# Kernel tuning notes

Hardware: AMD Instinct MI355X
Metric: run time of the kernel (lower is better)

The kernel has to match this reference:

```python
import jax, jax.numpy as jnp
import numpy as np

VOCAB, X_SIZE, H_SIZE, N_CLASSES = 50000, 300, 150, 5
DEPTH = 18                      # complete binary tree, N = 2^(DEPTH+1)-1 nodes
N_NODES = 2 ** (DEPTH + 1) - 1  # 524287
SCALE = 0.05                    # param init scale for numerical sanity


def setup_inputs() -> dict:
    key = jax.random.key(0)
    ks = jax.random.split(key, 8)
    return {
        "x_id": jax.random.randint(ks[0], (N_NODES,), 0, VOCAB, dtype=jnp.int32),
        "emb": jax.random.normal(ks[1], (VOCAB, X_SIZE), jnp.float32) * SCALE,
        "W_iou": jax.random.normal(ks[2], (X_SIZE, 3 * H_SIZE), jnp.float32) * SCALE,
        "U_iou": jax.random.normal(ks[3], (H_SIZE, 3 * H_SIZE), jnp.float32) * SCALE,
        "b_iou": jnp.zeros((3 * H_SIZE,), jnp.float32),
        "W_f": jax.random.normal(ks[4], (X_SIZE, H_SIZE), jnp.float32) * SCALE,
        "U_f": jax.random.normal(ks[5], (H_SIZE, H_SIZE), jnp.float32) * SCALE,
        "b_f": jnp.zeros((H_SIZE,), jnp.float32),
        "W_out": jax.random.normal(ks[6], (H_SIZE, N_CLASSES), jnp.float32) * SCALE,
        "b_out": jnp.zeros((N_CLASSES,), jnp.float32),
    }


def reference(x_id, emb, W_iou, U_iou, b_iou, W_f, U_f, b_f, W_out, b_out):
    # Child-Sum TreeLSTM propagated leaves->root over a complete binary tree
    # stored in heap layout: children of node i are 2i+1, 2i+2.
    N = x_id.shape[0]
    H = U_iou.shape[0]
    depth = int(np.log2(N + 1)) - 1

    x = emb[x_id]  # input_module: embedding lookup  [N, X]
    h = jnp.zeros((N, H), x.dtype)
    c = jnp.zeros((N, H), x.dtype)

    # level-batched topological propagation (19 static levels)
    for lvl in range(depth, -1, -1):
        s, e = 2 ** lvl - 1, 2 ** (lvl + 1) - 1  # node range of this level
        xl = x[s:e]                              # [n_l, X]
        if lvl == depth:  # leaves: zero child state
            h_sum = jnp.zeros((e - s, H), x.dtype)
            fc_sum = jnp.zeros((e - s, H), x.dtype)
        else:
            # children of consecutive nodes are contiguous: [2s+1, 2e+1)
            hc = h[2 * s + 1:2 * e + 1].reshape(e - s, 2, H)
            cc = c[2 * s + 1:2 * e + 1].reshape(e - s, 2, H)
            h_sum = hc.sum(axis=1)               # reduce: sum child h
            # per-child forget gate
            f = jax.nn.sigmoid((xl @ W_f)[:, None, :] + hc @ U_f + b_f)
            fc_sum = (f * cc).sum(axis=1)
        iou = xl @ W_iou + h_sum @ U_iou + b_iou  # [n_l, 3H]
        i, o, u = jnp.split(iou, 3, axis=-1)
        c_new = jax.nn.sigmoid(i) * jnp.tanh(u) + fc_sum
        h_new = jax.nn.sigmoid(o) * jnp.tanh(c_new)
        h = h.at[s:e].set(h_new)
        c = c.at[s:e].set(c_new)

    return h @ W_out + b_out  # output_module: Linear(H, C)  [N, C]
```

## Files before the change

### kernel.cpp

```cpp
#include <hip/hip_runtime.h>
#include <cstdint>

typedef _Float16 f16_t;
typedef __attribute__((ext_vector_type(8))) _Float16 f16x8;
typedef __attribute__((ext_vector_type(4))) _Float16 f16x4;
typedef __attribute__((ext_vector_type(4))) float f32x4;

#define HP      160
#define NCOL    640
#define KXP     320
#define NNODES  524287
#define LEAF_S  262143
#define LEAF_M  262144
#define NVOCAB  50000
#define AST     168

__device__ __forceinline__ float frcp(float x) { return __builtin_amdgcn_rcpf(x); }
__device__ __forceinline__ float sigf(float x) { return frcp(1.0f + __expf(-x)); }
__device__ __forceinline__ float tanhf_(float x) {
  return 1.0f - 2.0f * frcp(1.0f + __expf(2.0f * x));
}
__device__ __forceinline__ f16x8 zero8() {
  f16x8 z;
#pragma unroll
// ... 101 lines not shown
  }
}

__global__ void leafhc_kernel(const f16_t* __restrict__ P, f16_t* __restrict__ Hleaf,
                              f16_t* __restrict__ Cleaf) {
  int idx = blockIdx.x * 256 + threadIdx.x;
  if (idx >= NVOCAB * 80) return;
  int v = idx / 80, t = idx % 80;
  f16x8 pk = *(const f16x8*)&P[(long)v * NCOL + t * 8];
#pragma unroll
  for (int e = 0; e < 2; ++e) {
    float iv = (float)pk[e * 4 + 0], ov = (float)pk[e * 4 + 1], uv = (float)pk[e * 4 + 2];
    float cl = sigf(iv) * tanhf_(uv);
    float hl = sigf(ov) * tanhf_(cl);
    Hleaf[(long)v * HP + t * 2 + e] = (f16_t)hl;
    Cleaf[(long)v * HP + t * 2 + e] = (f16_t)cl;
  }
}

__global__ void oleaf_kernel(const f16_t* __restrict__ Hleaf, const float* __restrict__ W_out,
                             const float* __restrict__ b_out, float* __restrict__ Oleaf) {
  const int tid = threadIdx.x;
  const int row = blockIdx.x * 16 + (tid >> 4), l = tid & 15;
  if (row >= NVOCAB) return;
  float acc[5] = {0, 0, 0, 0, 0};
  for (int j = l; j < 150; j += 16) {
    float hv = (float)Hleaf[(long)row * HP + j];
#pragma unroll
    for (int m = 0; m < 5; ++m) acc[m] += hv * W_out[j * 5 + m];
  }
#pragma unroll
  for (int m = 0; m < 5; ++m) {
    float vv = acc[m];
    vv += __shfl_xor(vv, 1);
    vv += __shfl_xor(vv, 2);
    vv += __shfl_xor(vv, 4);
    vv += __shfl_xor(vv, 8);
    if (l == 0) Oleaf[(long)row * 8 + m] = vv + b_out[m];
  }
}

__global__ void leafout_kernel(const int* __restrict__ x_id, const float* __restrict__ Oleaf,
                               float* __restrict__ out) {
  int leaf = blockIdx.x * 256 + threadIdx.x;
  int xv = x_id[LEAF_S + leaf];
  const float* O = Oleaf + (long)xv * 8;
  float4 o4 = *(const float4*)O;
  float o5 = O[4];
  long base = ((long)LEAF_S + leaf) * 5;
  out[base + 0] = o4.x; out[base + 1] = o4.y; out[base + 2] = o4.z;
  out[base + 3] = o4.w; out[base + 4] = o5;
}

template <bool LEAF>
__global__ __launch_bounds__(256, 3) void fused_kernel(
    const int* __restrict__ x_id, const f16_t* __restrict__ P,
    const f16_t* __restrict__ UreT, const f16_t* __restrict__ Hc,
    const f16_t* __restrict__ Cc, f16_t* __restrict__ Hout,
    f16_t* __restrict__ Cout, const float* __restrict__ W_out,
    const float* __restrict__ b_out, float* __restrict__ out, int s1, int M1) {
  __shared__ __align__(16) f16_t A_sh[64 * AST];
  __shared__ __align__(16) f16_t A2_sh[32 * AST];
  __shared__ __align__(16) f16_t B_sh[128 * 40];
  __shared__ f16_t C_sh[32 * 160];
  const int tid = threadIdx.x;
  const int wid = tid >> 6, lane = tid & 63, l15 = lane & 15, q = lane >> 4;
  const int p0 = blockIdx.x * 32;
  const long childbase = 2L * s1 + 1 + 2 * p0;

#pragma unroll
  for (int i = 0; i < 5; ++i) {
    int ch = tid + 256 * i;
    int r = ch / 20, kc = (ch % 20) * 8;
    f16x8 v;
    if (LEAF) {
      int xv = x_id[childbase + r];
      v = *(const f16x8*)&Hc[(long)xv * HP + kc];
    } else {
      v = *(const f16x8*)&Hc[(long)(2 * p0 + r) * HP + kc];
    }
    *(f16x8*)&A_sh[r * AST + kc] = v;
  }
  __syncthreads();

  int xvp[2], xvl[2], xvr[2];
#pragma unroll
  for (int rr = 0; rr < 2; ++rr) {
    int pl = 8 * wid + 2 * q + rr;
    long pn = (long)s1 + p0 + pl;
    xvp[rr] = x_id[pn];
    if (LEAF) {
      xvl[rr] = x_id[childbase + 2 * pl];
      xvr[rr] = x_id[childbase + 2 * pl + 1];
    }
  }
  float oacc1[2][5] = {};

  for (int jt = 0; jt < 5; ++jt) {
    const int j0 = jt * 32;
    f32x4 acc[4][2];
#pragma unroll
    for (int g = 0; g < 4; ++g)
#pragma unroll
      for (int jh = 0; jh < 2; ++jh) acc[g][jh] = zero4();

    for (int kk = 0; kk < HP; kk += 32) {
#pragma unroll
// ... 106 lines not shown
          }
      }
      __syncthreads();
    }

    if (act2) {
#pragma unroll
      for (int rr = 0; rr < 2; ++rr) {
        const int r = rr * 2;
        const int lr0 = 16 * wid + q * 4 + r;
        const int pl = lr0 >> 1;
        const f16_t* Prp = P + (long)xvp2[rr] * NCOL;
#pragma unroll
        for (int jh = 0; jh < 2; ++jh) {
          const int j = j0 + jh * 16 + l15;
          f16x4 pp = *(const f16x4*)&Prp[j * 4];
          float ipre = (float)pp[0] + acc[0][jh][r] + acc[0][jh][r + 1];
          float opre = (float)pp[1] + acc[1][jh][r] + acc[1][jh][r + 1];
          float upre = (float)pp[2] + acc[2][jh][r] + acc[2][jh][r + 1];
          float pf   = (float)pp[3];
          float fl = sigf(pf + acc[3][jh][r]);
          float fr = sigf(pf + acc[3][jh][r + 1]);
          float clv = (float)C_sh[lr0 * 160 + j];
          float crv = (float)C_sh[(lr0 + 1) * 160 + j];
          float cn = sigf(ipre) * tanhf_(upre) + fl * clv + fr * crv;
          float hn = sigf(opre) * tanhf_(cn);
          Hout[(long)(p02 + pl) * HP + j] = (f16_t)hn;
          Cout[(long)(p02 + pl) * HP + j] = (f16_t)cn;
          int wbase = (j < 150) ? j * 5 : 0;
#pragma unroll
          for (int m = 0; m < 5; ++m) oacc2[rr][m] += hn * W_out[wbase + m];
        }
      }
    }
  }

  if (act2) {
#pragma unroll
    for (int rr = 0; rr < 2; ++rr) {
      int pl = 8 * wid + 2 * q + rr;
#pragma unroll
      for (int m = 0; m < 5; ++m) {
        float v = oacc2[rr][m];
        v += __shfl_xor(v, 1);
        v += __shfl_xor(v, 2);
        v += __shfl_xor(v, 4);
        v += __shfl_xor(v, 8);
        if (l15 == 0) out[((long)s2 + p02 + pl) * 5 + m] = v + b_out[m];
      }
    }
  }
}

__device__ __forceinline__ void level_tile(
    const int* __restrict__ x_id, const f16_t* __restrict__ P,
    const f16_t* __restrict__ UreT, const f16_t* __restrict__ h_child,
    const f16_t* __restrict__ c_child, f16_t* __restrict__ h_par,
    f16_t* __restrict__ c_par, const float* Wo, const float* __restrict__ b_out,
    float* __restrict__ out, int s, int M, int p0, f16_t* A_sh, f16_t* B_sh) {
  const int tid = threadIdx.x;
  const int wid = tid >> 6, lane = tid & 63, l15 = lane & 15, q = lane >> 4;
  int rowsValid = 2 * M - 2 * p0;
  if (rowsValid > 64) rowsValid = 64;

#pragma unroll
  for (int i = 0; i < 5; ++i) {
    int ch = tid + 256 * i;
    int r = ch / 20, kc = (ch % 20) * 8;
    f16x8 v;
    if (r < rowsValid) v = *(const f16x8*)&h_child[(long)(2 * p0 + r) * HP + kc];
    else v = zero8();
    *(f16x8*)&A_sh[r * 184 + kc] = v;
  }
  __syncthreads();

  int xvp[2]; long pnode[2]; int plg[2]; bool valid[2]; int lr0v[2];
#pragma unroll
  for (int rr = 0; rr < 2; ++rr) {
    int lr0 = 16 * wid + q * 4 + rr * 2;
    int pl = lr0 >> 1;
    valid[rr] = (p0 + pl) < M;
    long pn = (long)s + p0 + (valid[rr] ? pl : 0);
    pnode[rr] = pn; plg[rr] = p0 + pl; lr0v[rr] = lr0;
    xvp[rr] = x_id[pn];
  }

  float oacc[2][5];
#pragma unroll
  for (int rr = 0; rr < 2; ++rr)
#pragma unroll
    for (int m = 0; m < 5; ++m) oacc[rr][m] = 0.0f;

  for (int jt = 0; jt < 5; ++jt) {
    const int j0 = jt * 32;
    f32x4 acc[4][2];
#pragma unroll
    for (int g = 0; g < 4; ++g)
#pragma unroll
      for (int jh = 0; jh < 2; ++jh) acc[g][jh] = zero4();

    for (int kk = 0; kk < HP; kk += 32) {
#pragma unroll
      for (int i = 0; i < 2; ++i) {
        int ch = tid + 256 * i;
        int cidx = ch >> 2, kc = (ch & 3) * 8;
        int g = cidx >> 5, jj = cidx & 31;
        int col = g * HP + j0 + jj;
        *(f16x8*)&B_sh[cidx * 40 + kc] = *(const f16x8*)&UreT[col * HP + kk + kc];
      }
      __syncthreads();
      f16x8 af = *(const f16x8*)&A_sh[(16 * wid + l15) * 184 + kk + q * 8];
#pragma unroll
      for (int g = 0; g < 4; ++g)
#pragma unroll
        for (int jh = 0; jh < 2; ++jh) {
          f16x8 bfr = *(const f16x8*)&B_sh[(g * 32 + jh * 16 + l15) * 40 + q * 8];
          acc[g][jh] = __builtin_amdgcn_mfma_f32_16x16x32_f16(af, bfr, acc[g][jh], 0, 0, 0);
        }
      __syncthreads();
    }

#pragma unroll
    for (int rr = 0; rr < 2; ++rr) {
      const int r = rr * 2;
      const f16_t* Prp = P + (long)xvp[rr] * NCOL;
#pragma unroll
      for (int jh = 0; jh < 2; ++jh) {
        const int j = j0 + jh * 16 + l15;
        f16x4 pp = *(const f16x4*)&Prp[j * 4];
        float ipre = (float)pp[0] + acc[0][jh][r] + acc[0][jh][r + 1];
        float opre = (float)pp[1] + acc[1][jh][r] + acc[1][jh][r + 1];
        float upre = (float)pp[2] + acc[2][jh][r] + acc[2][jh][r + 1];
        float pf   = (float)pp[3];
        float fl = sigf(pf + acc[3][jh][r]);
        float fr = sigf(pf + acc[3][jh][r + 1]);
        float clv = valid[rr] ? (float)c_child[(long)(2 * p0 + lr0v[rr]) * HP + j] : 0.0f;
        float crv = valid[rr] ? (float)c_child[(long)(2 * p0 + lr0v[rr] + 1) * HP + j] : 0.0f;
        float cn = sigf(ipre) * tanhf_(upre) + fl * clv + fr * crv;
        float hn = sigf(opre) * tanhf_(cn);
        if (valid[rr]) {
          h_par[(long)plg[rr] * HP + j] = (f16_t)hn;
          c_par[(long)plg[rr] * HP + j] = (f16_t)cn;
        }
#pragma unroll
        for (int m = 0; m < 5; ++m) oacc[rr][m] += hn * Wo[j * 5 + m];
      }
    }
  }

#pragma unroll
  for (int rr = 0; rr < 2; ++rr) {
#pragma unroll
    for (int m = 0; m < 5; ++m) {
      float v = oacc[rr][m];
      v += __shfl_xor(v, 1);
      v += __shfl_xor(v, 2);
      v += __shfl_xor(v, 4);
      v += __shfl_xor(v, 8);
      if (l15 == 0 && valid[rr]) out[pnode[rr] * 5 + m] = v + b_out[m];
    }
  }
}

__global__ __launch_bounds__(256, 4) void tail_kernel(
    const int* __restrict__ x_id, const f16_t* __restrict__ P,
    const f16_t* __restrict__ UreT, f16_t* __restrict__ HA, f16_t* __restrict__ HB,
    f16_t* __restrict__ CA, f16_t* __restrict__ CB, const float* __restrict__ W_out,
    const float* __restrict__ b_out, float* __restrict__ out) {
  __shared__ __align__(16) f16_t A_sh[64 * 184];
  __shared__ __align__(16) f16_t B_sh[128 * 40];
  __shared__ float Wo[800];
  for (int i = threadIdx.x; i < 800; i += 256) Wo[i] = (i < 750) ? W_out[i] : 0.0f;
  for (int lvl = 5; lvl >= 0; --lvl) {
    int s = (1 << lvl) - 1, M = 1 << lvl;
    const f16_t* hc = ((lvl + 1) & 1) ? HA : HB;
    const f16_t* cc = ((lvl + 1) & 1) ? CA : CB;
    f16_t* hp = (lvl & 1) ? HA : HB;
    f16_t* cp = (lvl & 1) ? CA : CB;
    level_tile(x_id, P, UreT, hc, cc, hp, cp, Wo, b_out, out, s, M, 0, A_sh, B_sh);
    __syncthreads();
  }
}

extern "C" void kernel_launch(void* const* d_in, const int* in_sizes, int n_in,
                              void* d_out, int out_size, void* d_ws, size_t ws_size,
                              hipStream_t stream) {
  const int* x_id   = (const int*)d_in[0];
  const float* emb  = (const float*)d_in[1];
  const float* W_iou = (const float*)d_in[2];
  const float* U_iou = (const float*)d_in[3];
  const float* b_iou = (const float*)d_in[4];
  const float* W_f   = (const float*)d_in[5];
  const float* U_f   = (const float*)d_in[6];
  const float* b_f   = (const float*)d_in[7];
  const float* W_out = (const float*)d_in[8];
  const float* b_out = (const float*)d_in[9];
  float* out = (float*)d_out;
  char* ws = (char*)d_ws;

  f16_t* WreT  = (f16_t*)(ws + 0);
  f16_t* UreT  = (f16_t*)(ws + 409600);
  float* bre   = (float*)(ws + 614400);
  f16_t* P     = (f16_t*)(ws + 616960);
  f16_t* Hleaf = (f16_t*)(ws + 64616960);
  f16_t* Cleaf = (f16_t*)(ws + 80616960);
  float* Oleaf = (float*)(ws + 96616960);
  f16_t* HX    = (f16_t*)(ws + 98216960);
  f16_t* HY    = (f16_t*)(ws + 119188480);
  f16_t* CX    = (f16_t*)(ws + 140160000);
  f16_t* CY    = (f16_t*)(ws + 161131520);

  prep_params<<<1203, 256, 0, stream>>>(W_iou, U_iou, b_iou, W_f, U_f, b_f, WreT, UreT, bre);
  gemm_p<<<782, 256, 0, stream>>>(emb, WreT, bre, P);
  leafhc_kernel<<<15625, 256, 0, stream>>>(P, Hleaf, Cleaf);
  oleaf_kernel<<<3125, 256, 0, stream>>>(Hleaf, W_out, b_out, Oleaf);
  leafout_kernel<<<1024, 256, 0, stream>>>(x_id, Oleaf, out);

  fused_kernel<true><<<4096, 256, 0, stream>>>(x_id, P, UreT, Hleaf, Cleaf, HX, CX,
                                               W_out, b_out, out, (1 << 17) - 1, 1 << 17);
  fused_kernel<false><<<1024, 256, 0, stream>>>(x_id, P, UreT, HX, CX, HY, CY,
                                                W_out, b_out, out, (1 << 15) - 1, 1 << 15);
  fused_kernel<false><<<256, 256, 0, stream>>>(x_id, P, UreT, HY, CY, HX, CX,
                                               W_out, b_out, out, (1 << 13) - 1, 1 << 13);
  fused_kernel<false><<<64, 256, 0, stream>>>(x_id, P, UreT, HX, CX, HY, CY,
                                              W_out, b_out, out, (1 << 11) - 1, 1 << 11);
  fused_kernel<false><<<16, 256, 0, stream>>>(x_id, P, UreT, HY, CY, HX, CX,
                                              W_out, b_out, out, (1 << 9) - 1, 1 << 9);
  fused_kernel<false><<<4, 256, 0, stream>>>(x_id, P, UreT, HX, CX, HY, CY,
                                             W_out, b_out, out, (1 << 7) - 1, 1 << 7);
  tail_kernel<<<1, 256, 0, stream>>>(x_id, P, UreT, HX, HY, CX, CY, W_out, b_out, out);

  (void)in_sizes; (void)n_in; (void)out_size; (void)ws_size;
}
```

Measured before the change: 866.8 us.

## Add dedicated single-level kernel for level 17 and re-pair later levels

Result: faster. 823.0 us (-5.1%).

```diff
diff --git a/kernel.cpp b/kernel.cpp
--- a/kernel.cpp
+++ b/kernel.cpp
@@ -177,6 +177,111 @@
   out[base + 3] = o4.w; out[base + 4] = o5;
 }
 
+__global__ __launch_bounds__(256, 3) void level17_kernel(
+    const int* __restrict__ x_id, const f16_t* __restrict__ P,
+    const f16_t* __restrict__ UreT, const f16_t* __restrict__ Hleaf,
+    const f16_t* __restrict__ Cleaf, f16_t* __restrict__ Hout,
+    f16_t* __restrict__ Cout, const float* __restrict__ W_out,
+    const float* __restrict__ b_out, float* __restrict__ out) {
+  __shared__ __align__(16) f16_t A_sh[64 * AST];
+  __shared__ __align__(16) f16_t B_sh[128 * 40];
+  const int tid = threadIdx.x;
+  const int wid = tid >> 6, lane = tid & 63, l15 = lane & 15, q = lane >> 4;
+  const int p0 = blockIdx.x * 32;
+  const int s1 = (1 << 17) - 1;
+  const long childbase = 2L * s1 + 1 + 2 * p0;
+
+#pragma unroll
+  for (int i = 0; i < 5; ++i) {
+    int ch = tid + 256 * i;
+    int r = ch / 20, kc = (ch % 20) * 8;
+    int xv = x_id[childbase + r];
+    *(f16x8*)&A_sh[r * AST + kc] = *(const f16x8*)&Hleaf[(long)xv * HP + kc];
+  }
+  __syncthreads();
+
+  int xvp[2], xvl[2], xvr[2];
+#pragma unroll
+  for (int rr = 0; rr < 2; ++rr) {
+    int pl = 8 * wid + 2 * q + rr;
+    xvp[rr] = x_id[(long)s1 + p0 + pl];
+    xvl[rr] = x_id[childbase + 2 * pl];
+    xvr[rr] = x_id[childbase + 2 * pl + 1];
+  }
+  float oacc[2][5] = {};
+
+  for (int jt = 0; jt < 5; ++jt) {
+    const int j0 = jt * 32;
+    f32x4 acc[4][2];
+#pragma unroll
+    for (int g = 0; g < 4; ++g)
+#pragma unroll
+      for (int jh = 0; jh < 2; ++jh) acc[g][jh] = zero4();
+
+    for (int kk = 0; kk < HP; kk += 32) {
+#pragma unroll
+      for (int i = 0; i < 2; ++i) {
+        int ch = tid + 256 * i;
+        int cidx = ch >> 2, kc = (ch & 3) * 8;
+        int g = cidx >> 5, jj = cidx & 31;
+        int col = g * HP + j0 + jj;
+        *(f16x8*)&B_sh[cidx * 40 + kc] = *(const f16x8*)&UreT[col * HP + kk + kc];
+      }
+      __syncthreads();
+      f16x8 af = *(const f16x8*)&A_sh[(16 * wid + l15) * AST + kk + q * 8];
+#pragma unroll
+      for (int g = 0; g < 4; ++g)
+#pragma unroll
+        for (int jh = 0; jh < 2; ++jh) {
+          f16x8 bfr = *(const f16x8*)&B_sh[(g * 32 + jh * 16 + l15) * 40 + q * 8];
+          acc[g][jh] = __builtin_amdgcn_mfma_f32_16x16x32_f16(af, bfr, acc[g][jh], 0, 0, 0);
+        }
+      __syncthreads();
+    }
+
+#pragma unroll
+    for (int rr = 0; rr < 2; ++rr) {
+      const int r = rr * 2;
+      const int pl = 8 * wid + 2 * q + rr;
+      const f16_t* Prp = P + (long)xvp[rr] * NCOL;
+#pragma unroll
+      for (int jh = 0; jh < 2; ++jh) {
+        const int j = j0 + jh * 16 + l15;
+        f16x4 pp = *(const f16x4*)&Prp[j * 4];
+        float ipre = (float)pp[0] + acc[0][jh][r] + acc[0][jh][r + 1];
+        float opre = (float)pp[1] + acc[1][jh][r] + acc[1][jh][r + 1];
+        float upre = (float)pp[2] + acc[2][jh][r] + acc[2][jh][r + 1];
+        float pf   = (float)pp[3];
+        float fl = sigf(pf + acc[3][jh][r]);
+        float fr = sigf(pf + acc[3][jh][r + 1]);
+        float clv = (float)Cleaf[(long)xvl[rr] * HP + j];
+        float crv = (float)Cleaf[(long)xvr[rr] * HP + j];
+        float cn = sigf(ipre) * tanhf_(upre) + fl * clv + fr * crv;
+        float hn = sigf(opre) * tanhf_(cn);
+        Hout[(long)(p0 + pl) * HP + j] = (f16_t)hn;
+        Cout[(long)(p0 + pl) * HP + j] = (f16_t)cn;
+        int wbase = (j < 150) ? j * 5 : 0;
+#pragma unroll
+        for (int m = 0; m < 5; ++m) oacc[rr][m] += hn * W_out[wbase + m];
+      }
+    }
+  }
+
+#pragma unroll
+  for (int rr = 0; rr < 2; ++rr) {
+    int pl = 8 * wid + 2 * q + rr;
+#pragma unroll
+    for (int m = 0; m < 5; ++m) {
+      float v = oacc[rr][m];
+      v += __shfl_xor(v, 1);
+      v += __shfl_xor(v, 2);
+      v += __shfl_xor(v, 4);
+      v += __shfl_xor(v, 8);
+      if (l15 == 0) out[((long)s1 + p0 + pl) * 5 + m] = v + b_out[m];
+    }
+  }
+}
+
 template <bool LEAF>
 __global__ __launch_bounds__(256, 3) void fused_kernel(
     const int* __restrict__ x_id, const f16_t* __restrict__ P,
@@ -509,7 +614,7 @@
   __shared__ __align__(16) f16_t B_sh[128 * 40];
   __shared__ float Wo[800];
   for (int i = threadIdx.x; i < 800; i += 256) Wo[i] = (i < 750) ? W_out[i] : 0.0f;
-  for (int lvl = 5; lvl >= 0; --lvl) {
+  for (int lvl = 4; lvl >= 0; --lvl) {
     int s = (1 << lvl) - 1, M = 1 << lvl;
     const f16_t* hc = ((lvl + 1) & 1) ? HA : HB;
     const f16_t* cc = ((lvl + 1) & 1) ? CA : CB;
@@ -543,10 +648,22 @@
   f16_t* Hleaf = (f16_t*)(ws + 64616960);
   f16_t* Cleaf = (f16_t*)(ws + 80616960);
   float* Oleaf = (float*)(ws + 96616960);
-  f16_t* HX    = (f16_t*)(ws + 98216960);
-  f16_t* HY    = (f16_t*)(ws + 119188480);
-  f16_t* CX    = (f16_t*)(ws + 140160000);
-  f16_t* CY    = (f16_t*)(ws + 161131520);
+  f16_t* H17   = (f16_t*)(ws + 96616960);
+  f16_t* C17   = (f16_t*)(ws + 138560000);
+  f16_t* H15 = (f16_t*)(ws + 64616960);
+  f16_t* C15 = (f16_t*)(ws + 75102720);
+  f16_t* H13 = (f16_t*)(ws + 96616960);
+  f16_t* C13 = (f16_t*)(ws + 99238400);
+  f16_t* H11 = (f16_t*)(ws + 64616960);
+  f16_t* C11 = (f16_t*)(ws + 65272320);
+  f16_t* H9  = (f16_t*)(ws + 96616960);
+  f16_t* C9  = (f16_t*)(ws + 96780800);
+  f16_t* H7  = (f16_t*)(ws + 64616960);
+  f16_t* C7  = (f16_t*)(ws + 64657920);
+  f16_t* H5  = (f16_t*)(ws + 96616960);
+  f16_t* C5  = (f16_t*)(ws + 96627200);
+  f16_t* HSc = (f16_t*)(ws + 64616960);
+  f16_t* CSc = (f16_t*)(ws + 64627200);
 
   prep_params<<<1203, 256, 0, stream>>>(W_iou, U_iou, b_iou, W_f, U_f, b_f, WreT, UreT, bre);
   gemm_p<<<782, 256, 0, stream>>>(emb, WreT, bre, P);
@@ -554,19 +671,21 @@
   oleaf_kernel<<<3125, 256, 0, stream>>>(Hleaf, W_out, b_out, Oleaf);
   leafout_kernel<<<1024, 256, 0, stream>>>(x_id, Oleaf, out);
 
-  fused_kernel<true><<<4096, 256, 0, stream>>>(x_id, P, UreT, Hleaf, Cleaf, HX, CX,
-                                               W_out, b_out, out, (1 << 17) - 1, 1 << 17);
-  fused_kernel<false><<<1024, 256, 0, stream>>>(x_id, P, UreT, HX, CX, HY, CY,
-                                                W_out, b_out, out, (1 << 15) - 1, 1 << 15);
-  fused_kernel<false><<<256, 256, 0, stream>>>(x_id, P, UreT, HY, CY, HX, CX,
-                                               W_out, b_out, out, (1 << 13) - 1, 1 << 13);
-  fused_kernel<false><<<64, 256, 0, stream>>>(x_id, P, UreT, HX, CX, HY, CY,
-                                              W_out, b_out, out, (1 << 11) - 1, 1 << 11);
-  fused_kernel<false><<<16, 256, 0, stream>>>(x_id, P, UreT, HY, CY, HX, CX,
-                                              W_out, b_out, out, (1 << 9) - 1, 1 << 9);
-  fused_kernel<false><<<4, 256, 0, stream>>>(x_id, P, UreT, HX, CX, HY, CY,
-                                             W_out, b_out, out, (1 << 7) - 1, 1 << 7);
-  tail_kernel<<<1, 256, 0, stream>>>(x_id, P, UreT, HX, HY, CX, CY, W_out, b_out, out);
+  level17_kernel<<<4096, 256, 0, stream>>>(x_id, P, UreT, Hleaf, Cleaf, H17, C17,
+                                           W_out, b_out, out);
+  fused_kernel<false><<<2048, 256, 0, stream>>>(x_id, P, UreT, H17, C17, H15, C15,
+                                                W_out, b_out, out, (1 << 16) - 1, 1 << 16);
+  fused_kernel<false><<<512, 256, 0, stream>>>(x_id, P, UreT, H15, C15, H13, C13,
+                                               W_out, b_out, out, (1 << 14) - 1, 1 << 14);
+  fused_kernel<false><<<128, 256, 0, stream>>>(x_id, P, UreT, H13, C13, H11, C11,
+                                               W_out, b_out, out, (1 << 12) - 1, 1 << 12);
+  fused_kernel<false><<<32, 256, 0, stream>>>(x_id, P, UreT, H11, C11, H9, C9,
+                                              W_out, b_out, out, (1 << 10) - 1, 1 << 10);
+  fused_kernel<false><<<8, 256, 0, stream>>>(x_id, P, UreT, H9, C9, H7, C7,
+                                             W_out, b_out, out, (1 << 8) - 1, 1 << 8);
+  fused_kernel<false><<<2, 256, 0, stream>>>(x_id, P, UreT, H7, C7, H5, C5,
+                                             W_out, b_out, out, (1 << 6) - 1, 1 << 6);
+  tail_kernel<<<1, 256, 0, stream>>>(x_id, P, UreT, H5, HSc, C5, CSc, W_out, b_out, out);
 
   (void)in_sizes; (void)n_in; (void)out_size; (void)ws_size;
 }
```

## Split tree levels into per-level kernels with node-per-block small-level path

Applied to the files above, without the earlier changes.

After: 991.3 us. 1.14x slower.

```diff
diff --git a/kernel.cpp b/kernel.cpp
--- a/kernel.cpp
+++ b/kernel.cpp
@@ -177,6 +177,111 @@
   out[base + 3] = o4.w; out[base + 4] = o5;
 }
 
+__global__ __launch_bounds__(256, 3) void level17_kernel(
+    const int* __restrict__ x_id, const f16_t* __restrict__ P,
+    const f16_t* __restrict__ UreT, const f16_t* __restrict__ Hleaf,
+    const f16_t* __restrict__ Cleaf, f16_t* __restrict__ Hout,
+    f16_t* __restrict__ Cout, const float* __restrict__ W_out,
+    const float* __restrict__ b_out, float* __restrict__ out) {
+  __shared__ __align__(16) f16_t A_sh[64 * AST];
+  __shared__ __align__(16) f16_t B_sh[128 * 40];
+  const int tid = threadIdx.x;
+  const int wid = tid >> 6, lane = tid & 63, l15 = lane & 15, q = lane >> 4;
+  const int p0 = blockIdx.x * 32;
+  const int s1 = (1 << 17) - 1;
+  const long childbase = 2L * s1 + 1 + 2 * p0;
+
+#pragma unroll
+  for (int i = 0; i < 5; ++i) {
+    int ch = tid + 256 * i;
+    int r = ch / 20, kc = (ch % 20) * 8;
+    int xv = x_id[childbase + r];
+    *(f16x8*)&A_sh[r * AST + kc] = *(const f16x8*)&Hleaf[(long)xv * HP + kc];
+  }
+  __syncthreads();
+
+  int xvp[2], xvl[2], xvr[2];
+#pragma unroll
+  for (int rr = 0; rr < 2; ++rr) {
+    int pl = 8 * wid + 2 * q + rr;
+    xvp[rr] = x_id[(long)s1 + p0 + pl];
+    xvl[rr] = x_id[childbase + 2 * pl];
+    xvr[rr] = x_id[childbase + 2 * pl + 1];
+  }
+  float oacc[2][5] = {};
+
+  for (int jt = 0; jt < 5; ++jt) {
+    const int j0 = jt * 32;
+    f32x4 acc[4][2];
+#pragma unroll
+    for (int g = 0; g < 4; ++g)
+#pragma unroll
+      for (int jh = 0; jh < 2; ++jh) acc[g][jh] = zero4();
+
+    for (int kk = 0; kk < HP; kk += 32) {
+#pragma unroll
+      for (int i = 0; i < 2; ++i) {
+        int ch = tid + 256 * i;
+        int cidx = ch >> 2, kc = (ch & 3) * 8;
+        int g = cidx >> 5, jj = cidx & 31;
+        int col = g * HP + j0 + jj;
+        *(f16x8*)&B_sh[cidx * 40 + kc] = *(const f16x8*)&UreT[col * HP + kk + kc];
+      }
+      __syncthreads();
+      f16x8 af = *(const f16x8*)&A_sh[(16 * wid + l15) * AST + kk + q * 8];
+#pragma unroll
+      for (int g = 0; g < 4; ++g)
+#pragma unroll
+        for (int jh = 0; jh < 2; ++jh) {
+          f16x8 bfr = *(const f16x8*)&B_sh[(g * 32 + jh * 16 + l15) * 40 + q * 8];
+          acc[g][jh] = __builtin_amdgcn_mfma_f32_16x16x32_f16(af, bfr, acc[g][jh], 0, 0, 0);
+        }
+      __syncthreads();
+    }
+
+#pragma unroll
+    for (int rr = 0; rr < 2; ++rr) {
+      const int r = rr * 2;
+      const int pl = 8 * wid + 2 * q + rr;
+      const f16_t* Prp = P + (long)xvp[rr] * NCOL;
+#pragma unroll
+      for (int jh = 0; jh < 2; ++jh) {
+        const int j = j0 + jh * 16 + l15;
+        f16x4 pp = *(const f16x4*)&Prp[j * 4];
+        float ipre = (float)pp[0] + acc[0][jh][r] + acc[0][jh][r + 1];
+        float opre = (float)pp[1] + acc[1][jh][r] + acc[1][jh][r + 1];
+        float upre = (float)pp[2] + acc[2][jh][r] + acc[2][jh][r + 1];
+        float pf   = (float)pp[3];
+        float fl = sigf(pf + acc[3][jh][r]);
+        float fr = sigf(pf + acc[3][jh][r + 1]);
+        float clv = (float)Cleaf[(long)xvl[rr] * HP + j];
+        float crv = (float)Cleaf[(long)xvr[rr] * HP + j];
+        float cn = sigf(ipre) * tanhf_(upre) + fl * clv + fr * crv;
+        float hn = sigf(opre) * tanhf_(cn);
+        Hout[(long)(p0 + pl) * HP + j] = (f16_t)hn;
+        Cout[(long)(p0 + pl) * HP + j] = (f16_t)cn;
+        int wbase = (j < 150) ? j * 5 : 0;
+#pragma unroll
+        for (int m = 0; m < 5; ++m) oacc[rr][m] += hn * W_out[wbase + m];
+      }
+    }
+  }
+
+#pragma unroll
+  for (int rr = 0; rr < 2; ++rr) {
+    int pl = 8 * wid + 2 * q + rr;
+#pragma unroll
+    for (int m = 0; m < 5; ++m) {
+      float v = oacc[rr][m];
+      v += __shfl_xor(v, 1);
+      v += __shfl_xor(v, 2);
+      v += __shfl_xor(v, 4);
+      v += __shfl_xor(v, 8);
+      if (l15 == 0) out[((long)s1 + p0 + pl) * 5 + m] = v + b_out[m];
+    }
+  }
+}
+
 template <bool LEAF>
 __global__ __launch_bounds__(256, 3) void fused_kernel(
     const int* __restrict__ x_id, const f16_t* __restrict__ P,
@@ -390,133 +495,78 @@
   }
 }
 
-__device__ __forceinline__ void level_tile(
+__global__ __launch_bounds__(256) void small_level(
     const int* __restrict__ x_id, const f16_t* __restrict__ P,
-    const f16_t* __restrict__ UreT, const f16_t* __restrict__ h_child,
-    const f16_t* __restrict__ c_child, f16_t* __restrict__ h_par,
-    f16_t* __restrict__ c_par, const float* Wo, const float* __restrict__ b_out,
-    float* __restrict__ out, int s, int M, int p0, f16_t* A_sh, f16_t* B_sh) {
+    const f16_t* __restrict__ UreT, const f16_t* __restrict__ Hc,
+    const f16_t* __restrict__ Cc, f16_t* __restrict__ Hp, f16_t* __restrict__ Cp,
+    const float* __restrict__ W_out, const float* __restrict__ b_out,
+    float* __restrict__ out, int s) {
+  __shared__ __align__(16) f16_t hlr[320];
+  __shared__ float partial[4][5];
   const int tid = threadIdx.x;
-  const int wid = tid >> 6, lane = tid & 63, l15 = lane & 15, q = lane >> 4;
-  int rowsValid = 2 * M - 2 * p0;
-  if (rowsValid > 64) rowsValid = 64;
-
-#pragma unroll
-  for (int i = 0; i < 5; ++i) {
-    int ch = tid + 256 * i;
-    int r = ch / 20, kc = (ch % 20) * 8;
-    f16x8 v;
-    if (r < rowsValid) v = *(const f16x8*)&h_child[(long)(2 * p0 + r) * HP + kc];
-    else v = zero8();
-    *(f16x8*)&A_sh[r * 184 + kc] = v;
-  }
+  const int p = blockIdx.x;
+  const long cb = (long)(2 * p) * HP;
+
+  if (tid < 40) *(f16x8*)&hlr[tid * 8] = *(const f16x8*)&Hc[cb + tid * 8];
   __syncthreads();
 
-  int xvp[2]; long pnode[2]; int plg[2]; bool valid[2]; int lr0v[2];
-#pragma unroll
-  for (int rr = 0; rr < 2; ++rr) {
-    int lr0 = 16 * wid + q * 4 + rr * 2;
-    int pl = lr0 >> 1;
-    valid[rr] = (p0 + pl) < M;
-    long pn = (long)s + p0 + (valid[rr] ? pl : 0);
-    pnode[rr] = pn; plg[rr] = p0 + pl; lr0v[rr] = lr0;
-    xvp[rr] = x_id[pn];
-  }
-
-  float oacc[2][5];
-#pragma unroll
-  for (int rr = 0; rr < 2; ++rr)
-#pragma unroll
-    for (int m = 0; m < 5; ++m) oacc[rr][m] = 0.0f;
-
-  for (int jt = 0; jt < 5; ++jt) {
-    const int j0 = jt * 32;
-    f32x4 acc[4][2];
-#pragma unroll
-    for (int g = 0; g < 4; ++g)
-#pragma unroll
-      for (int jh = 0; jh < 2; ++jh) acc[g][jh] = zero4();
-
-    for (int kk = 0; kk < HP; kk += 32) {
-#pragma unroll
-      for (int i = 0; i < 2; ++i) {
-        int ch = tid + 256 * i;
-        int cidx = ch >> 2, kc = (ch & 3) * 8;
-        int g = cidx >> 5, jj = cidx & 31;
-        int col = g * HP + j0 + jj;
-        *(f16x8*)&B_sh[cidx * 40 + kc] = *(const f16x8*)&UreT[col * HP + kk + kc];
-      }
-      __syncthreads();
-      f16x8 af = *(const f16x8*)&A_sh[(16 * wid + l15) * 184 + kk + q * 8];
-#pragma unroll
-      for (int g = 0; g < 4; ++g)
-#pragma unroll
-        for (int jh = 0; jh < 2; ++jh) {
-          f16x8 bfr = *(const f16x8*)&B_sh[(g * 32 + jh * 16 + l15) * 40 + q * 8];
-          acc[g][jh] = __builtin_amdgcn_mfma_f32_16x16x32_f16(af, bfr, acc[g][jh], 0, 0, 0);
-        }
-      __syncthreads();
-    }
-
-#pragma unroll
-    for (int rr = 0; rr < 2; ++rr) {
-      const int r = rr * 2;
-      const f16_t* Prp = P + (long)xvp[rr] * NCOL;
-#pragma unroll
-      for (int jh = 0; jh < 2; ++jh) {
-        const int j = j0 + jh * 16 + l15;
-        f16x4 pp = *(const f16x4*)&Prp[j * 4];
-        float ipre = (float)pp[0] + acc[0][jh][r] + acc[0][jh][r + 1];
-        float opre = (float)pp[1] + acc[1][jh][r] + acc[1][jh][r + 1];
-        float upre = (float)pp[2] + acc[2][jh][r] + acc[2][jh][r + 1];
-        float pf   = (float)pp[3];
-        float fl = sigf(pf + acc[3][jh][r]);
-        float fr = sigf(pf + acc[3][jh][r + 1]);
-        float clv = valid[rr] ? (float)c_child[(long)(2 * p0 + lr0v[rr]) * HP + j] : 0.0f;
-        float crv = valid[rr] ? (float)c_child[(long)(2 * p0 + lr0v[rr] + 1) * HP + j] : 0.0f;
-        float cn = sigf(ipre) * tanhf_(upre) + fl * clv + fr * crv;
-        float hn = sigf(opre) * tanhf_(cn);
-        if (valid[rr]) {
-          h_par[(long)plg[rr] * HP + j] = (f16_t)hn;
-          c_par[(long)plg[rr] * HP + j] = (f16_t)cn;
-        }
-#pragma unroll
-        for (int m = 0; m < 5; ++m) oacc[rr][m] += hn * Wo[j * 5 + m];
-      }
-    }
-  }
-
-#pragma unroll
-  for (int rr = 0; rr < 2; ++rr) {
-#pragma unroll
-    for (int m = 0; m < 5; ++m) {
-      float v = oacc[rr][m];
-      v += __shfl_xor(v, 1);
-      v += __shfl_xor(v, 2);
-      v += __shfl_xor(v, 4);
-      v += __shfl_xor(v, 8);
-      if (l15 == 0 && valid[rr]) out[pnode[rr] * 5 + m] = v + b_out[m];
-    }
-  }
-}
-
-__global__ __launch_bounds__(256, 4) void tail_kernel(
-    const int* __restrict__ x_id, const f16_t* __restrict__ P,
-    const f16_t* __restrict__ UreT, f16_t* __restrict__ HA, f16_t* __restrict__ HB,
-    f16_t* __restrict__ CA, f16_t* __restrict__ CB, const float* __restrict__ W_out,
-    const float* __restrict__ b_out, float* __restrict__ out) {
-  __shared__ __align__(16) f16_t A_sh[64 * 184];
-  __shared__ __align__(16) f16_t B_sh[128 * 40];
-  __shared__ float Wo[800];
-  for (int i = threadIdx.x; i < 800; i += 256) Wo[i] = (i < 750) ? W_out[i] : 0.0f;
-  for (int lvl = 5; lvl >= 0; --lvl) {
-    int s = (1 << lvl) - 1, M = 1 << lvl;
-    const f16_t* hc = ((lvl + 1) & 1) ? HA : HB;
-    const f16_t* cc = ((lvl + 1) & 1) ? CA : CB;
-    f16_t* hp = (lvl & 1) ? HA : HB;
-    f16_t* cp = (lvl & 1) ? CA : CB;
-    level_tile(x_id, P, UreT, hc, cc, hp, cp, Wo, b_out, out, s, M, 0, A_sh, B_sh);
-    __syncthreads();
+  const int j = tid;
+  float ai = 0.f, ao = 0.f, au = 0.f, afl = 0.f, afr = 0.f;
+  float hn = 0.f;
+  float contrib[5] = {0.f, 0.f, 0.f, 0.f, 0.f};
+  if (j < HP) {
+    const f16_t* Ui = &UreT[(long)(0 * HP + j) * HP];
+    const f16_t* Uo = &UreT[(long)(1 * HP + j) * HP];
+    const f16_t* Uu = &UreT[(long)(2 * HP + j) * HP];
+    const f16_t* Uf = &UreT[(long)(3 * HP + j) * HP];
+#pragma unroll 5
+    for (int k8 = 0; k8 < 19; ++k8) {
+      f16x8 hl8 = *(const f16x8*)&hlr[k8 * 8];
+      f16x8 hr8 = *(const f16x8*)&hlr[160 + k8 * 8];
+      f16x8 ui8 = *(const f16x8*)&Ui[k8 * 8];
+      f16x8 uo8 = *(const f16x8*)&Uo[k8 * 8];
+      f16x8 uu8 = *(const f16x8*)&Uu[k8 * 8];
+      f16x8 uf8 = *(const f16x8*)&Uf[k8 * 8];
+#pragma unroll
+      for (int e = 0; e < 8; ++e) {
+        float hlv = (float)hl8[e], hrv = (float)hr8[e];
+        float hsv = hlv + hrv;
+        ai  += hsv * (float)ui8[e];
+        ao  += hsv * (float)uo8[e];
+        au  += hsv * (float)uu8[e];
+        afl += hlv * (float)uf8[e];
+        afr += hrv * (float)uf8[e];
+      }
+    }
+    int xv = x_id[(long)s + p];
+    f16x4 pp = *(const f16x4*)&P[(long)xv * NCOL + j * 4];
+    float ipre = (float)pp[0] + ai;
+    float opre = (float)pp[1] + ao;
+    float upre = (float)pp[2] + au;
+    float pf   = (float)pp[3];
+    float fl = sigf(pf + afl), fr = sigf(pf + afr);
+    float clv = (float)Cc[cb + j];
+    float crv = (float)Cc[cb + HP + j];
+    float cn = sigf(ipre) * tanhf_(upre) + fl * clv + fr * crv;
+    hn = sigf(opre) * tanhf_(cn);
+    Hp[(long)p * HP + j] = (f16_t)hn;
+    Cp[(long)p * HP + j] = (f16_t)cn;
+    int wbase = (j < 150) ? j * 5 : 0;
+#pragma unroll
+    for (int m = 0; m < 5; ++m) contrib[m] = hn * W_out[wbase + m];
+  }
+  const int w = tid >> 6, l = tid & 63;
+#pragma unroll
+  for (int m = 0; m < 5; ++m) {
+    float v = contrib[m];
+    v += __shfl_xor(v, 1);  v += __shfl_xor(v, 2);  v += __shfl_xor(v, 4);
+    v += __shfl_xor(v, 8);  v += __shfl_xor(v, 16); v += __shfl_xor(v, 32);
+    if (l == 0) partial[w][m] = v;
+  }
+  __syncthreads();
+  if (tid < 5) {
+    float v = partial[0][tid] + partial[1][tid] + partial[2][tid] + partial[3][tid];
+    out[((long)s + p) * 5 + tid] = v + b_out[tid];
   }
 }
 
@@ -543,10 +593,19 @@
   f16_t* Hleaf = (f16_t*)(ws + 64616960);
   f16_t* Cleaf = (f16_t*)(ws + 80616960);
   float* Oleaf = (float*)(ws + 96616960);
-  f16_t* HX    = (f16_t*)(ws + 98216960);
-  f16_t* HY    = (f16_t*)(ws + 119188480);
-  f16_t* CX    = (f16_t*)(ws + 140160000);
-  f16_t* CY    = (f16_t*)(ws + 161131520);
+  f16_t* H17   = (f16_t*)(ws + 96616960);
+  f16_t* C17   = (f16_t*)(ws + 138560000);
+  f16_t* H15 = (f16_t*)(ws + 64616960);
+  f16_t* C15 = (f16_t*)(ws + 75102720);
+  f16_t* H13 = (f16_t*)(ws + 96616960);
+  f16_t* C13 = (f16_t*)(ws + 99238400);
+  char* vb = ws + 85588480;
+  f16_t* VH[13]; f16_t* VC[13];
+  for (int L = 12; L >= 0; --L) {
+    size_t rows = (size_t)1 << L;
+    VH[L] = (f16_t*)vb; vb += rows * 320;
+    VC[L] = (f16_t*)vb; vb += rows * 320;
+  }
 
   prep_params<<<1203, 256, 0, stream>>>(W_iou, U_iou, b_iou, W_f, U_f, b_f, WreT, UreT, bre);
   gemm_p<<<782, 256, 0, stream>>>(emb, WreT, bre, P);
@@ -554,19 +613,19 @@
   oleaf_kernel<<<3125, 256, 0, stream>>>(Hleaf, W_out, b_out, Oleaf);
   leafout_kernel<<<1024, 256, 0, stream>>>(x_id, Oleaf, out);
 
-  fused_kernel<true><<<4096, 256, 0, stream>>>(x_id, P, UreT, Hleaf, Cleaf, HX, CX,
-                                               W_out, b_out, out, (1 << 17) - 1, 1 << 17);
-  fused_kernel<false><<<1024, 256, 0, stream>>>(x_id, P, UreT, HX, CX, HY, CY,
-                                                W_out, b_out, out, (1 << 15) - 1, 1 << 15);
-  fused_kernel<false><<<256, 256, 0, stream>>>(x_id, P, UreT, HY, CY, HX, CX,
-                                               W_out, b_out, out, (1 << 13) - 1, 1 << 13);
-  fused_kernel<false><<<64, 256, 0, stream>>>(x_id, P, UreT, HX, CX, HY, CY,
-                                              W_out, b_out, out, (1 << 11) - 1, 1 << 11);
-  fused_kernel<false><<<16, 256, 0, stream>>>(x_id, P, UreT, HY, CY, HX, CX,
-                                              W_out, b_out, out, (1 << 9) - 1, 1 << 9);
-  fused_kernel<false><<<4, 256, 0, stream>>>(x_id, P, UreT, HX, CX, HY, CY,
-                                             W_out, b_out, out, (1 << 7) - 1, 1 << 7);
-  tail_kernel<<<1, 256, 0, stream>>>(x_id, P, UreT, HX, HY, CX, CY, W_out, b_out, out);
+  level17_kernel<<<4096, 256, 0, stream>>>(x_id, P, UreT, Hleaf, Cleaf, H17, C17,
+                                           W_out, b_out, out);
+  fused_kernel<false><<<2048, 256, 0, stream>>>(x_id, P, UreT, H17, C17, H15, C15,
+                                                W_out, b_out, out, (1 << 16) - 1, 1 << 16);
+  fused_kernel<false><<<512, 256, 0, stream>>>(x_id, P, UreT, H15, C15, H13, C13,
+                                               W_out, b_out, out, (1 << 14) - 1, 1 << 14);
+  small_level<<<4096, 256, 0, stream>>>(x_id, P, UreT, H13, C13, VH[12], VC[12],
+                                        W_out, b_out, out, (1 << 12) - 1);
+  for (int L = 11; L >= 0; --L) {
+    small_level<<<(1 << L), 256, 0, stream>>>(x_id, P, UreT, VH[L + 1], VC[L + 1],
+                                              VH[L], VC[L], W_out, b_out, out,
+                                              (1 << L) - 1);
+  }
 
   (void)in_sizes; (void)n_in; (void)out_size; (void)ws_size;
 }
```

## Replace two-level fused kernels with per-level kernels staging full UreT tile in LDS

Applied to the files above, without the earlier changes.

New measurement: 884.4 us. 1.02x slower.

```diff
diff --git a/kernel.cpp b/kernel.cpp
--- a/kernel.cpp
+++ b/kernel.cpp
@@ -178,6 +178,142 @@
 }
 
 template <bool LEAF>
+__device__ __forceinline__ void level_tile_fk(
+    const int* __restrict__ x_id, const f16_t* __restrict__ P,
+    const f16_t* __restrict__ UreT, const f16_t* __restrict__ Hc,
+    const f16_t* __restrict__ Cc, f16_t* __restrict__ Hp, f16_t* __restrict__ Cp,
+    const float* __restrict__ W_out, const float* __restrict__ b_out,
+    float* __restrict__ out, int s, int M, int p0, f16_t* A_sh, f16_t* B_sh) {
+  const int tid = threadIdx.x;
+  const int wid = tid >> 6, lane = tid & 63, l15 = lane & 15, q = lane >> 4;
+  const long childbase = 2L * s + 1 + 2 * p0;
+  int rowsValid = 2 * M - 2 * p0;
+  if (rowsValid > 64) rowsValid = 64;
+
+#pragma unroll
+  for (int i = 0; i < 5; ++i) {
+    int ch = tid + 256 * i;
+    int r = ch / 20, kc = (ch % 20) * 8;
+    f16x8 v;
+    if (LEAF) {
+      int xv = x_id[childbase + r];
+      v = *(const f16x8*)&Hc[(long)xv * HP + kc];
+    } else {
+      v = (r < rowsValid) ? *(const f16x8*)&Hc[(long)(2 * p0 + r) * HP + kc] : zero8();
+    }
+    *(f16x8*)&A_sh[r * AST + kc] = v;
+  }
+
+  int xvp[2], xvl[2], xvr[2]; bool valid[2];
+#pragma unroll
+  for (int rr = 0; rr < 2; ++rr) {
+    int pl = 8 * wid + 2 * q + rr;
+    valid[rr] = (p0 + pl) < M;
+    long pn = (long)s + p0 + (valid[rr] ? pl : 0);
+    xvp[rr] = x_id[pn];
+    if (LEAF) {
+      xvl[rr] = x_id[childbase + 2 * pl];
+      xvr[rr] = x_id[childbase + 2 * pl + 1];
+    }
+  }
+  float oacc[2][5] = {};
+
+  for (int jt = 0; jt < 5; ++jt) {
+    const int j0 = jt * 32;
+#pragma unroll
+    for (int i = 0; i < 10; ++i) {
+      int ch = tid + 256 * i;
+      int r = ch / 20, kc = (ch % 20) * 8;
+      int col = (r >> 5) * HP + j0 + (r & 31);
+      *(f16x8*)&B_sh[r * AST + kc] = *(const f16x8*)&UreT[(long)col * HP + kc];
+    }
+    __syncthreads();
+
+    f32x4 acc[4][2];
+#pragma unroll
+    for (int g = 0; g < 4; ++g)
+#pragma unroll
+      for (int jh = 0; jh < 2; ++jh) acc[g][jh] = zero4();
+
+#pragma unroll
+    for (int kk = 0; kk < HP; kk += 32) {
+      f16x8 af = *(const f16x8*)&A_sh[(16 * wid + l15) * AST + kk + q * 8];
+#pragma unroll
+      for (int g = 0; g < 4; ++g)
+#pragma unroll
+        for (int jh = 0; jh < 2; ++jh) {
+          f16x8 bfr = *(const f16x8*)&B_sh[(g * 32 + jh * 16 + l15) * AST + kk + q * 8];
+          acc[g][jh] = __builtin_amdgcn_mfma_f32_16x16x32_f16(af, bfr, acc[g][jh], 0, 0, 0);
+        }
+    }
+    __syncthreads();
+
+#pragma unroll
+    for (int rr = 0; rr < 2; ++rr) {
+      const int r = rr * 2;
+      const int lr0 = 16 * wid + q * 4 + r;
+      const int pl = lr0 >> 1;
+      const f16_t* Prp = P + (long)xvp[rr] * NCOL;
+#pragma unroll
+      for (int jh = 0; jh < 2; ++jh) {
+        const int j = j0 + jh * 16 + l15;
+        f16x4 pp = *(const f16x4*)&Prp[j * 4];
+        float ipre = (float)pp[0] + acc[0][jh][r] + acc[0][jh][r + 1];
+        float opre = (float)pp[1] + acc[1][jh][r] + acc[1][jh][r + 1];
+        float upre = (float)pp[2] + acc[2][jh][r] + acc[2][jh][r + 1];
+        float pf   = (float)pp[3];
+        float fl = sigf(pf + acc[3][jh][r]);
+        float fr = sigf(pf + acc[3][jh][r + 1]);
+        float clv, crv;
+        if (LEAF) {
+          clv = (float)Cc[(long)xvl[rr] * HP + j];
+          crv = (float)Cc[(long)xvr[rr] * HP + j];
+        } else {
+          clv = valid[rr] ? (float)Cc[(long)(2 * p0 + lr0) * HP + j] : 0.0f;
+          crv = valid[rr] ? (float)Cc[(long)(2 * p0 + lr0 + 1) * HP + j] : 0.0f;
+        }
+        float cn = sigf(ipre) * tanhf_(upre) + fl * clv + fr * crv;
+        float hn = sigf(opre) * tanhf_(cn);
+        if (valid[rr]) {
+          Hp[(long)(p0 + pl) * HP + j] = (f16_t)hn;
+          Cp[(long)(p0 + pl) * HP + j] = (f16_t)cn;
+        }
+        int wbase = (j < 150) ? j * 5 : 0;
+#pragma unroll
+        for (int m = 0; m < 5; ++m) oacc[rr][m] += hn * W_out[wbase + m];
+      }
+    }
+  }
+
+#pragma unroll
+  for (int rr = 0; rr < 2; ++rr) {
+    int pl = 8 * wid + 2 * q + rr;
+#pragma unroll
+    for (int m = 0; m < 5; ++m) {
+      float v = oacc[rr][m];
+      v += __shfl_xor(v, 1);
+      v += __shfl_xor(v, 2);
+      v += __shfl_xor(v, 4);
+      v += __shfl_xor(v, 8);
+      if (l15 == 0 && valid[rr]) out[((long)s + p0 + pl) * 5 + m] = v + b_out[m];
+    }
+  }
+}
+
+template <bool LEAF>
+__global__ __launch_bounds__(256, 2) void level_kernel(
+    const int* __restrict__ x_id, const f16_t* __restrict__ P,
+    const f16_t* __restrict__ UreT, const f16_t* __restrict__ Hc,
+    const f16_t* __restrict__ Cc, f16_t* __restrict__ Hout,
+    f16_t* __restrict__ Cout, const float* __restrict__ W_out,
+    const float* __restrict__ b_out, float* __restrict__ out, int s, int M) {
+  __shared__ __align__(16) f16_t A_sh[64 * AST];
+  __shared__ __align__(16) f16_t B_sh[128 * AST];
+  level_tile_fk<LEAF>(x_id, P, UreT, Hc, Cc, Hout, Cout, W_out, b_out, out,
+                      s, M, blockIdx.x * 32, A_sh, B_sh);
+}
+
+template <bool LEAF>
 __global__ __launch_bounds__(256, 3) void fused_kernel(
     const int* __restrict__ x_id, const f16_t* __restrict__ P,
     const f16_t* __restrict__ UreT, const f16_t* __restrict__ Hc,
@@ -390,132 +526,21 @@
   }
 }
 
-__device__ __forceinline__ void level_tile(
-    const int* __restrict__ x_id, const f16_t* __restrict__ P,
-    const f16_t* __restrict__ UreT, const f16_t* __restrict__ h_child,
-    const f16_t* __restrict__ c_child, f16_t* __restrict__ h_par,
-    f16_t* __restrict__ c_par, const float* Wo, const float* __restrict__ b_out,
-    float* __restrict__ out, int s, int M, int p0, f16_t* A_sh, f16_t* B_sh) {
-  const int tid = threadIdx.x;
-  const int wid = tid >> 6, lane = tid & 63, l15 = lane & 15, q = lane >> 4;
-  int rowsValid = 2 * M - 2 * p0;
-  if (rowsValid > 64) rowsValid = 64;
-
-#pragma unroll
-  for (int i = 0; i < 5; ++i) {
-    int ch = tid + 256 * i;
-    int r = ch / 20, kc = (ch % 20) * 8;
-    f16x8 v;
-    if (r < rowsValid) v = *(const f16x8*)&h_child[(long)(2 * p0 + r) * HP + kc];
-    else v = zero8();
-    *(f16x8*)&A_sh[r * 184 + kc] = v;
-  }
-  __syncthreads();
-
-  int xvp[2]; long pnode[2]; int plg[2]; bool valid[2]; int lr0v[2];
-#pragma unroll
-  for (int rr = 0; rr < 2; ++rr) {
-    int lr0 = 16 * wid + q * 4 + rr * 2;
-    int pl = lr0 >> 1;
-    valid[rr] = (p0 + pl) < M;
-    long pn = (long)s + p0 + (valid[rr] ? pl : 0);
-    pnode[rr] = pn; plg[rr] = p0 + pl; lr0v[rr] = lr0;
-    xvp[rr] = x_id[pn];
-  }
-
-  float oacc[2][5];
-#pragma unroll
-  for (int rr = 0; rr < 2; ++rr)
-#pragma unroll
-    for (int m = 0; m < 5; ++m) oacc[rr][m] = 0.0f;
-
-  for (int jt = 0; jt < 5; ++jt) {
-    const int j0 = jt * 32;
-    f32x4 acc[4][2];
-#pragma unroll
-    for (int g = 0; g < 4; ++g)
-#pragma unroll
-      for (int jh = 0; jh < 2; ++jh) acc[g][jh] = zero4();
-
-    for (int kk = 0; kk < HP; kk += 32) {
-#pragma unroll
-      for (int i = 0; i < 2; ++i) {
-        int ch = tid + 256 * i;
-        int cidx = ch >> 2, kc = (ch & 3) * 8;
-        int g = cidx >> 5, jj = cidx & 31;
-        int col = g * HP + j0 + jj;
-        *(f16x8*)&B_sh[cidx * 40 + kc] = *(const f16x8*)&UreT[col * HP + kk + kc];
-      }
-      __syncthreads();
-      f16x8 af = *(const f16x8*)&A_sh[(16 * wid + l15) * 184 + kk + q * 8];
-#pragma unroll
-      for (int g = 0; g < 4; ++g)
-#pragma unroll
-        for (int jh = 0; jh < 2; ++jh) {
-          f16x8 bfr = *(const f16x8*)&B_sh[(g * 32 + jh * 16 + l15) * 40 + q * 8];
-          acc[g][jh] = __builtin_amdgcn_mfma_f32_16x16x32_f16(af, bfr, acc[g][jh], 0, 0, 0);
-        }
-      __syncthreads();
-    }
-
-#pragma unroll
-    for (int rr = 0; rr < 2; ++rr) {
-      const int r = rr * 2;
-      const f16_t* Prp = P + (long)xvp[rr] * NCOL;
-#pragma unroll
-      for (int jh = 0; jh < 2; ++jh) {
-        const int j = j0 + jh * 16 + l15;
-        f16x4 pp = *(const f16x4*)&Prp[j * 4];
-        float ipre = (float)pp[0] + acc[0][jh][r] + acc[0][jh][r + 1];
-        float opre = (float)pp[1] + acc[1][jh][r] + acc[1][jh][r + 1];
-        float upre = (float)pp[2] + acc[2][jh][r] + acc[2][jh][r + 1];
-        float pf   = (float)pp[3];
-        float fl = sigf(pf + acc[3][jh][r]);
-        float fr = sigf(pf + acc[3][jh][r + 1]);
-        float clv = valid[rr] ? (float)c_child[(long)(2 * p0 + lr0v[rr]) * HP + j] : 0.0f;
-        float crv = valid[rr] ? (float)c_child[(long)(2 * p0 + lr0v[rr] + 1) * HP + j] : 0.0f;
-        float cn = sigf(ipre) * tanhf_(upre) + fl * clv + fr * crv;
-        float hn = sigf(opre) * tanhf_(cn);
-        if (valid[rr]) {
-          h_par[(long)plg[rr] * HP + j] = (f16_t)hn;
-          c_par[(long)plg[rr] * HP + j] = (f16_t)cn;
-        }
-#pragma unroll
-        for (int m = 0; m < 5; ++m) oacc[rr][m] += hn * Wo[j * 5 + m];
-      }
-    }
-  }
-
-#pragma unroll
-  for (int rr = 0; rr < 2; ++rr) {
-#pragma unroll
-    for (int m = 0; m < 5; ++m) {
-      float v = oacc[rr][m];
-      v += __shfl_xor(v, 1);
-      v += __shfl_xor(v, 2);
-      v += __shfl_xor(v, 4);
-      v += __shfl_xor(v, 8);
-      if (l15 == 0 && valid[rr]) out[pnode[rr] * 5 + m] = v + b_out[m];
-    }
-  }
-}
-
-__global__ __launch_bounds__(256, 4) void tail_kernel(
+__global__ __launch_bounds__(256, 2) void tail_fk(
     const int* __restrict__ x_id, const f16_t* __restrict__ P,
     const f16_t* __restrict__ UreT, f16_t* __restrict__ HA, f16_t* __restrict__ HB,
     f16_t* __restrict__ CA, f16_t* __restrict__ CB, const float* __restrict__ W_out,
     const float* __restrict__ b_out, float* __restrict__ out) {
-  __shared__ __align__(16) f16_t A_sh[64 * 184];
-  __shared__ __align__(16) f16_t B_sh[128 * 40];
-  __shared__ float Wo[800];
-  for (int i = threadIdx.x; i < 800; i += 256) Wo[i] = (i < 750) ? W_out[i] : 0.0f;
+  __shared__ __align__(16) f16_t A_sh[64 * AST];
+  __shared__ __align__(16) f16_t B_sh[128 * AST];
   for (int lvl = 5; lvl >= 0; --lvl) {
     int s = (1 << lvl) - 1, M = 1 << lvl;
     const f16_t* hc = ((lvl + 1) & 1) ? HA : HB;
     const f16_t* cc = ((lvl + 1) & 1) ? CA : CB;
     f16_t* hp = (lvl & 1) ? HA : HB;
     f16_t* cp = (lvl & 1) ? CA : CB;
-    level_tile(x_id, P, UreT, hc, cc, hp, cp, Wo, b_out, out, s, M, 0, A_sh, B_sh);
+    level_tile_fk<false>(x_id, P, UreT, hc, cc, hp, cp, W_out, b_out, out,
+                         s, M, 0, A_sh, B_sh);
     __syncthreads();
   }
 }
@@ -543,10 +568,19 @@
   f16_t* Hleaf = (f16_t*)(ws + 64616960);
   f16_t* Cleaf = (f16_t*)(ws + 80616960);
   float* Oleaf = (float*)(ws + 96616960);
-  f16_t* HX    = (f16_t*)(ws + 98216960);
-  f16_t* HY    = (f16_t*)(ws + 119188480);
-  f16_t* CX    = (f16_t*)(ws + 140160000);
-  f16_t* CY    = (f16_t*)(ws + 161131520);
+  f16_t* H17   = (f16_t*)(ws + 96616960);
+  f16_t* C17   = (f16_t*)(ws + 138560000);
+  f16_t* H15   = (f16_t*)(ws + 64616960);
+  f16_t* C15   = (f16_t*)(ws + 75102720);
+  f16_t* HL[15]; f16_t* CL[15];
+  for (int L = 14; L >= 6; --L) {
+    size_t rows = (size_t)1 << L;
+    char* base = ((L & 1) == 0) ? (ws + 96616960) : (ws + 85588480);
+    HL[L] = (f16_t*)base;
+    CL[L] = (f16_t*)(base + rows * 320);
+  }
+  f16_t* HT = (f16_t*)(ws + 85588480);
+  f16_t* CT = (f16_t*)(ws + 85598720);
 
   prep_params<<<1203, 256, 0, stream>>>(W_iou, U_iou, b_iou, W_f, U_f, b_f, WreT, UreT, bre);
   gemm_p<<<782, 256, 0, stream>>>(emb, WreT, bre, P);
@@ -554,19 +588,22 @@
   oleaf_kernel<<<3125, 256, 0, stream>>>(Hleaf, W_out, b_out, Oleaf);
   leafout_kernel<<<1024, 256, 0, stream>>>(x_id, Oleaf, out);
 
-  fused_kernel<true><<<4096, 256, 0, stream>>>(x_id, P, UreT, Hleaf, Cleaf, HX, CX,
-                                               W_out, b_out, out, (1 << 17) - 1, 1 << 17);
-  fused_kernel<false><<<1024, 256, 0, stream>>>(x_id, P, UreT, HX, CX, HY, CY,
-                                                W_out, b_out, out, (1 << 15) - 1, 1 << 15);
-  fused_kernel<false><<<256, 256, 0, stream>>>(x_id, P, UreT, HY, CY, HX, CX,
-                                               W_out, b_out, out, (1 << 13) - 1, 1 << 13);
-  fused_kernel<false><<<64, 256, 0, stream>>>(x_id, P, UreT, HX, CX, HY, CY,
-                                              W_out, b_out, out, (1 << 11) - 1, 1 << 11);
-  fused_kernel<false><<<16, 256, 0, stream>>>(x_id, P, UreT, HY, CY, HX, CX,
-                                              W_out, b_out, out, (1 << 9) - 1, 1 << 9);
-  fused_kernel<false><<<4, 256, 0, stream>>>(x_id, P, UreT, HX, CX, HY, CY,
-                                             W_out, b_out, out, (1 << 7) - 1, 1 << 7);
-  tail_kernel<<<1, 256, 0, stream>>>(x_id, P, UreT, HX, HY, CX, CY, W_out, b_out, out);
+  level_kernel<true><<<4096, 256, 0, stream>>>(x_id, P, UreT, Hleaf, Cleaf,
+                                               H17, C17, W_out, b_out, out,
+                                               (1 << 17) - 1, 1 << 17);
+  fused_kernel<false><<<2048, 256, 0, stream>>>(x_id, P, UreT, H17, C17, H15, C15,
+                                                W_out, b_out, out, (1 << 16) - 1, 1 << 16);
+  {
+    const f16_t* hc = H15; const f16_t* cc = C15;
+    for (int L = 14; L >= 6; --L) {
+      int M = 1 << L;
+      level_kernel<false><<<(M + 31) / 32, 256, 0, stream>>>(
+          x_id, P, UreT, hc, cc, HL[L], CL[L], W_out, b_out, out, M - 1, M);
+      hc = HL[L]; cc = CL[L];
+    }
+  }
+  tail_fk<<<1, 256, 0, stream>>>(x_id, P, UreT, HT, HL[6], CT, CL[6],
+                                 W_out, b_out, out);
 
   (void)in_sizes; (void)n_in; (void)out_size; (void)ws_size;
 }
```
